# Optimization experiments

Hardware: AMD Instinct MI355X
Metric: run time of the kernel (lower is better)

## Reference

```python
import jax, jax.numpy as jnp
import numpy as np

V, E, H, B, S = 32000, 512, 1024, 128, 64
EPS = 0.05


def setup_inputs() -> dict:
    key = jax.random.key(0)
    ks = jax.random.split(key, 4)
    s = 0.02
    return {
        "emb": jax.random.normal(ks[0], (V, E), jnp.float32) * s,
        "w_ih": jax.random.normal(ks[1], (3 * H, E), jnp.float32) * s,
        "w_hh": jax.random.normal(ks[2], (3 * H, H), jnp.float32) * s,
        "b_ih": jnp.zeros((3 * H,), jnp.float32),
        "b_hh": jnp.zeros((3 * H,), jnp.float32),
        "w_dist": jax.random.normal(ks[3], (V, H), jnp.float32) * s,
        "b_dist": jnp.zeros((V,), jnp.float32),
    }


def reference(emb, w_ih, w_hh, b_ih, b_hh, w_dist, b_dist):
    base = jax.random.key(42)
    log_unif = -jnp.log(jnp.float32(V))  # log prob of uniform draw
    rows = jnp.arange(B)

    def step(carry, t):
        h, x = carry
        # PyTorch GRUCell math
        gx = x @ w_ih.T + b_ih            # [B, 3H]
        gh = h @ w_hh.T + b_hh            # [B, 3H]
        xr, xz, xn = jnp.split(gx, 3, axis=1)
        hr, hz, hn = jnp.split(gh, 3, axis=1)
        r = jax.nn.sigmoid(xr + hr)
        z = jax.nn.sigmoid(xz + hz)
        n = jnp.tanh(xn + r * hn)
        h_new = (1.0 - z) * n + z * h     # [B, H]

        dist = jax.nn.log_softmax(h_new @ w_dist.T + b_dist, axis=-1)  # [B, V]
        dist_sg = jax.lax.stop_gradient(dist)  # .detach() in torch

        k = jax.random.fold_in(base, t)
        k1, k2 = jax.random.split(k)
        # epsilon-exploration: replace whole row by uniform log-prob
        draw = jax.random.uniform(k1, (B,)) <= EPS
        dist_new = jnp.where(draw[:, None], log_unif, dist_sg)
        # Gumbel-max categorical sampling: argmax(dist_new - log(-log U))
        gumbel = -jnp.log(-jnp.log(jax.random.uniform(k2, (B, V))))
        sampled = jnp.argmax(dist_new + gumbel, axis=1)  # [B] int

        logprob = dist[rows, sampled]                                # [B]
        onp = jnp.clip(jnp.exp(dist_sg[rows, sampled]), 1e-8, 1.0)
        offp = jnp.clip(jnp.exp(dist_new[rows, sampled]), 1e-8, 1.0)
        correction = onp / offp
        prob_mean = jnp.mean(jnp.exp(dist_sg), axis=0)               # [V]

        x_next = emb[sampled]  # feed sampled token back in
        return (h_new, x_next), (sampled, correction, logprob, prob_mean)

    h0 = jnp.zeros((B, H), emb.dtype)
    x0 = jnp.broadcast_to(emb[0], (B, E))  # embedding of zero_input
    _, (samp, corr, lp, probs) = jax.lax.scan(step, (h0, x0), jnp.arange(S))
    # stack along time then transpose to [B, S] like torch.cat(..., 1)
    return samp.T, corr.T, lp.T, probs
```

## Files before the change

### kernel.cpp

```cpp
#include <hip/hip_runtime.h>
#include <cstdint>
#include <cmath>

#define V 32000
#define E 512
#define H 1024
#define B 128
#define S 64
#define NCHUNK 8
#define CHUNK 4000
#define PSTRIDE 250
#define BS (B*S)
#define PS 40
#define NEG_HUGE (-3.0e38f)

typedef __attribute__((ext_vector_type(8))) short short8;
typedef __attribute__((ext_vector_type(4))) float f32x4;

#define TFR(x0, x1, r) { x0 += x1; x1 = ((x1) << (r)) | ((x1) >> (32 - (r))); x1 ^= x0; }

__host__ __device__ inline void tf2x32(uint32_t k0, uint32_t k1, uint32_t &x0, uint32_t &x1) {
  uint32_t ks2 = k0 ^ k1 ^ 0x1BD11BDAu;
  x0 += k0; x1 += k1;
  TFR(x0,x1,13) TFR(x0,x1,15) TFR(x0,x1,26) TFR(x0,x1,6)
  x0 += k1;  x1 += ks2 + 1u;
  TFR(x0,x1,17) TFR(x0,x1,29) TFR(x0,x1,16) TFR(x0,x1,24)
  x0 += ks2; x1 += k0 + 2u;
  TFR(x0,x1,13) TFR(x0,x1,15) TFR(x0,x1,26) TFR(x0,x1,6)
  x0 += k0;  x1 += k1 + 3u;
  TFR(x0,x1,17) TFR(x0,x1,29) TFR(x0,x1,16) TFR(x0,x1,24)
  x0 += k1;  x1 += ks2 + 4u;
  TFR(x0,x1,13) TFR(x0,x1,15) TFR(x0,x1,26) TFR(x0,x1,6)
  x0 += ks2; x1 += k0 + 5u;
}

__device__ __forceinline__ uint32_t tf_bits32(uint32_t ka, uint32_t kb, uint32_t idx) {
  uint32_t x0 = 0u, x1 = idx;
  tf2x32(ka, kb, x0, x1);
  return x0 ^ x1;
}

__device__ __forceinline__ float bits_to_unif(uint32_t b) {
  return __uint_as_float((b >> 9) | 0x3f800000u) - 1.0f;
}

__device__ __forceinline__ float sigmoidf_(float x) { return 1.0f / (1.0f + expf(-x)); }

__device__ __forceinline__ ushort f2bf(float f) {
  uint32_t u = __float_as_uint(f);
  uint32_t r = u + 0x7FFFu + ((u >> 16) & 1u);
  return (ushort)(r >> 16);
}
__device__ __forceinline__ float bf2f(ushort h) { return __uint_as_float(((uint32_t)h) << 16); }

template<int BM, int BN, int BK, int TM, int TN>
__device__ void gemm_tile(const float* __restrict__ A, const float* __restrict__ Wt,
                          const float* __restrict__ bias, float* __restrict__ C,
                          int N, int K, int mblk, int nblk)
{
  constexpr int WP = BN + 4;
  __shared__ __align__(16) float As[BK][BM];
  __shared__ __align__(16) float Ws[BK][WP];
  const int tid = threadIdx.x;
  constexpr int TX = BN / TN;
  constexpr int TY = BM / TM;
  static_assert(TX * TY == 256, "bad tiling");
  const int tx = tid % TX, ty = tid / TX;
  const int n0 = tx * TN, m0 = ty * TM;

  float acc[TM][TN];
#pragma unroll
  for (int i = 0; i < TM; ++i)
#pragma unroll
    for (int j = 0; j < TN; ++j) acc[i][j] = 0.0f;

  constexpr int NA = (BM * BK / 4) / 256;
  constexpr int NW = (BN * BK / 4) / 256;
  static_assert(NA >= 1 && NW >= 1, "tile too small");

  for (int k0 = 0; k0 < K; k0 += BK) {
    __syncthreads();
#pragma unroll
    for (int q = 0; q < NA; ++q) {
      int idx = q * 256 + tid;
      int m = idx / (BK / 4), c = idx % (BK / 4);
      float4 v = *(const float4*)&A[(size_t)(mblk + m) * K + k0 + 4 * c];
      As[4*c+0][m] = v.x; As[4*c+1][m] = v.y; As[4*c+2][m] = v.z; As[4*c+3][m] = v.w;
    }
#pragma unroll
    for (int q = 0; q < NW; ++q) {
      int idx = q * 256 + tid;
      int n = idx / (BK / 4), c = idx % (BK / 4);
      float4 v = *(const float4*)&Wt[(size_t)(nblk + n) * K + k0 + 4 * c];
      Ws[4*c+0][n] = v.x; Ws[4*c+1][n] = v.y; Ws[4*c+2][n] = v.z; Ws[4*c+3][n] = v.w;
    }
    __syncthreads();
#pragma unroll
    for (int k = 0; k < BK; ++k) {
      float a[TM], w[TN];
#pragma unroll
      for (int i = 0; i < TM; ++i) a[i] = As[k][m0 + i];
#pragma unroll
      for (int j = 0; j < TN; ++j) w[j] = Ws[k][n0 + j];
#pragma unroll
      for (int i = 0; i < TM; ++i)
#pragma unroll
        for (int j = 0; j < TN; ++j) acc[i][j] += a[i] * w[j];
    }
  }
#pragma unroll
  for (int i = 0; i < TM; ++i)
#pragma unroll
    for (int j = 0; j < TN; ++j)
      C[(size_t)(mblk + m0 + i) * N + nblk + n0 + j] = acc[i][j] + bias[nblk + n0 + j];
}

__global__ __launch_bounds__(256) void gemm_dist_k(const float* __restrict__ h,
    const float* __restrict__ w_dist, const float* __restrict__ b_dist,
    float* __restrict__ logits)
{
  gemm_tile<128, 64, 16, 8, 4>(h, w_dist, b_dist, logits, V, H, 0, blockIdx.x * 64);
}

__global__ __launch_bounds__(256) void gemm_gru_k(const float* __restrict__ x,
    const float* __restrict__ h, const float* __restrict__ w_ih, const float* __restrict__ w_hh,
    const float* __restrict__ b_ih, const float* __restrict__ b_hh,
    float* __restrict__ gx, float* __restrict__ gh)
{
  int b = blockIdx.x;
  if (b < 96) {
    int rb = b & 1, cb = b >> 1;
    gemm_tile<64, 64, 16, 4, 4>(x, w_ih, b_ih, gx, 3 * H, E, rb * 64, cb * 64);
  } else {
    b -= 96;
    int rb = b & 1, cb = b >> 1;
    gemm_tile<64, 64, 16, 4, 4>(h, w_hh, b_hh, gh, 3 * H, H, rb * 64, cb * 64);
  }
}

__global__ __launch_bounds__(256) void wsplit_k(const float* __restrict__ w,
    ushort* __restrict__ whi, ushort* __restrict__ wlo, int n4)
{
  int idx = blockIdx.x * 256 + threadIdx.x;
  if (idx >= n4) return;
  size_t i = (size_t)idx * 4;
  float4 v = *(const float4*)&w[i];
  ushort h0 = f2bf(v.x), h1 = f2bf(v.y), h2 = f2bf(v.z), h3 = f2bf(v.w);
  ushort l0 = f2bf(v.x - bf2f(h0)), l1 = f2bf(v.y - bf2f(h1));
  ushort l2 = f2bf(v.z - bf2f(h2)), l3 = f2bf(v.w - bf2f(h3));
  ushort4 hv = {h0, h1, h2, h3}, lv = {l0, l1, l2, l3};
  *(ushort4*)&whi[i] = hv;
  *(ushort4*)&wlo[i] = lv;
}

__global__ __launch_bounds__(256) void gru_gates_k(const float* __restrict__ gx,
    const float* __restrict__ gh, float* __restrict__ h,
    ushort* __restrict__ hhi, ushort* __restrict__ hlo)
{
  int idx = blockIdx.x * 256 + threadIdx.x;
  int b = idx >> 10, j = idx & 1023;
  const float* gxb = gx + (size_t)b * 3 * H;
  const float* ghb = gh + (size_t)b * 3 * H;
  float r = sigmoidf_(gxb[j] + ghb[j]);
  float z = sigmoidf_(gxb[H + j] + ghb[H + j]);
  float n = tanhf(gxb[2 * H + j] + r * ghb[2 * H + j]);
  float hn = (1.0f - z) * n + z * h[idx];
  h[idx] = hn;
  ushort hi = f2bf(hn);
  hhi[idx] = hi;
  hlo[idx] = f2bf(hn - bf2f(hi));
}

__global__ __launch_bounds__(512) void gemm_dist_mfma(const ushort* __restrict__ hhi,
    const ushort* __restrict__ hlo, const ushort* __restrict__ whi,
    const ushort* __restrict__ wlo, const float* __restrict__ b_dist,
    float* __restrict__ logits,
    float* __restrict__ pm, float* __restrict__ ps,
    float* __restrict__ pbest, int* __restrict__ pidx,
    uint32_t k1a, uint32_t k1b, uint32_t k2a, uint32_t k2b)
{
  __shared__ ushort Ah[128 * PS], Al[128 * PS], Wh[128 * PS], Wl[128 * PS];
  __shared__ float rm[2 * 128], rs[2 * 128], rb_[2 * 128];
  __shared__ int   ri[2 * 128];
  __shared__ uint32_t sdraw[128];
  const int tid = threadIdx.x;
  const int wave = tid >> 6, lane = tid & 63;
  const int wm = (wave & 3) * 32;
  const int wn = (wave >> 2) * 64;
  const int nblk = blockIdx.x * 128;
  const int l15 = lane & 15;
  const int q = lane >> 4;
  const int q8 = q * 8;

  if (tid < 128)
    sdraw[tid] = (bits_to_unif(tf_bits32(k1a, k1b, (uint32_t)tid)) <= 0.05f) ? 1u : 0u;

  f32x4 acc[2][4] = {};
  const int sr = tid >> 2, sc = (tid & 3) * 8;

  for (int k0 = 0; k0 < 1024; k0 += 32) {
    __syncthreads();
    uint4 va = *(const uint4*)&hhi[(size_t)sr * 1024 + k0 + sc];
    uint4 vb = *(const uint4*)&hlo[(size_t)sr * 1024 + k0 + sc];
    uint4 vc = *(const uint4*)&whi[(size_t)(nblk + sr) * 1024 + k0 + sc];
    uint4 vd = *(const uint4*)&wlo[(size_t)(nblk + sr) * 1024 + k0 + sc];
    *(uint4*)&Ah[sr * PS + sc] = va;
    *(uint4*)&Al[sr * PS + sc] = vb;
    *(uint4*)&Wh[sr * PS + sc] = vc;
    *(uint4*)&Wl[sr * PS + sc] = vd;
    __syncthreads();

    short8 ah[2], al[2], wh[4], wl[4];
#pragma unroll
    for (int mt = 0; mt < 2; ++mt) {
      int row = wm + mt * 16 + l15;
      ah[mt] = *(const short8*)&Ah[row * PS + q8];
      al[mt] = *(const short8*)&Al[row * PS + q8];
    }
#pragma unroll
    for (int nt = 0; nt < 4; ++nt) {
      int row = wn + nt * 16 + l15;
      wh[nt] = *(const short8*)&Wh[row * PS + q8];
      wl[nt] = *(const short8*)&Wl[row * PS + q8];
    }
#pragma unroll
    for (int mt = 0; mt < 2; ++mt)
#pragma unroll
      for (int nt = 0; nt < 4; ++nt) {
        acc[mt][nt] = __builtin_amdgcn_mfma_f32_16x16x32_bf16(ah[mt], wh[nt], acc[mt][nt], 0, 0, 0);
        acc[mt][nt] = __builtin_amdgcn_mfma_f32_16x16x32_bf16(al[mt], wh[nt], acc[mt][nt], 0, 0, 0);
        acc[mt][nt] = __builtin_amdgcn_mfma_f32_16x16x32_bf16(ah[mt], wl[nt], acc[mt][nt], 0, 0, 0);
      }
  }

  float bv[4];
#pragma unroll
  for (int nt = 0; nt < 4; ++nt) bv[nt] = b_dist[nblk + wn + nt * 16 + l15];

  const float LOGU = -logf((float)V);
#pragma unroll
  for (int mt = 0; mt < 2; ++mt) {
#pragma unroll
    for (int reg = 0; reg < 4; ++reg) {
      const int r = wm + mt * 16 + q * 4 + reg;
      const bool draw = sdraw[r] != 0u;
      float m0 = NEG_HUGE, s0 = 0.0f, best = NEG_HUGE;
      int bi = 2147483647;
#pragma unroll
      for (int nt = 0; nt < 4; ++nt) {
        const int col = nblk + wn + nt * 16 + l15;
        float a = acc[mt][nt][reg] + bv[nt];
        logits[(size_t)r * V + col] = a;
        if (a > m0) { s0 = s0 * expf(m0 - a) + 1.0f; m0 = a; } else { s0 += expf(a - m0); }
        uint32_t bits = tf_bits32(k2a, k2b, (uint32_t)(r * V + col));
        float g = -logf(-logf(bits_to_unif(bits)));
        float key = draw ? (LOGU + g) : (a + g);
        if (key > best) { best = key; bi = col; }
      }
#pragma unroll
      for (int off = 1; off < 16; off <<= 1) {
        float mo = __shfl_xor(m0, off);
        float so = __shfl_xor(s0, off);
        float M = fmaxf(m0, mo);
        s0 = s0 * expf(m0 - M) + so * expf(mo - M);
        m0 = M;
        float bo = __shfl_xor(best, off);
        int io = __shfl_xor(bi, off);
        if (bo > best || (bo == best && io < bi)) { best = bo; bi = io; }
      }
      if (l15 == 0) {
        const int slot = (wave >> 2) * 128 + r;
        rm[slot] = m0; rs[slot] = s0; rb_[slot] = best; ri[slot] = bi;
      }
    }
  }
  __syncthreads();
  if (tid < 128) {
    float ma = rm[tid], sa = rs[tid], mb = rm[128 + tid], sb = rs[128 + tid];
    float M = fmaxf(ma, mb);
    float s = sa * expf(ma - M) + sb * expf(mb - M);
    pm[tid * PSTRIDE + blockIdx.x] = M;
    ps[tid * PSTRIDE + blockIdx.x] = s;
    float va = rb_[tid], vb = rb_[128 + tid];
    int ia = ri[tid], ib = ri[128 + tid];
    if (vb > va || (vb == va && ib < ia)) { va = vb; ia = ib; }
    pbest[tid * PSTRIDE + blockIdx.x] = va;
    pidx[tid * PSTRIDE + blockIdx.x] = ia;
  }
}

__device__ void gemm64_bf16x3(const ushort* __restrict__ Ahi_g, const ushort* __restrict__ Alo_g,
    const ushort* __restrict__ Whi_g, const ushort* __restrict__ Wlo_g,
    const float* __restrict__ bias, float* __restrict__ C,
    int N, int K, int mblk, int nblk)
{
  __shared__ ushort Ah[64 * PS], Al[64 * PS], Wh[64 * PS], Wl[64 * PS];
  const int tid = threadIdx.x;
  const int wave = tid >> 6, lane = tid & 63;
  const int wm = (wave & 1) * 32, wn = (wave >> 1) * 32;
  const int l15 = lane & 15, q8 = (lane >> 4) * 8;
  const int sr = tid >> 2, sc = (tid & 3) * 8;

  f32x4 acc[2][2] = {};

  for (int k0 = 0; k0 < K; k0 += 32) {
    __syncthreads();
    uint4 va = *(const uint4*)&Ahi_g[(size_t)(mblk + sr) * K + k0 + sc];
    uint4 vb = *(const uint4*)&Alo_g[(size_t)(mblk + sr) * K + k0 + sc];
    uint4 vc = *(const uint4*)&Whi_g[(size_t)(nblk + sr) * K + k0 + sc];
    uint4 vd = *(const uint4*)&Wlo_g[(size_t)(nblk + sr) * K + k0 + sc];
    *(uint4*)&Ah[sr * PS + sc] = va;
    *(uint4*)&Al[sr * PS + sc] = vb;
    *(uint4*)&Wh[sr * PS + sc] = vc;
    *(uint4*)&Wl[sr * PS + sc] = vd;
    __syncthreads();

    short8 ah[2], al[2], wh[2], wl[2];
#pragma unroll
    for (int mt = 0; mt < 2; ++mt) {
      int row = wm + mt * 16 + l15;
      ah[mt] = *(const short8*)&Ah[row * PS + q8];
      al[mt] = *(const short8*)&Al[row * PS + q8];
    }
#pragma unroll
    for (int nt = 0; nt < 2; ++nt) {
      int row = wn + nt * 16 + l15;
      wh[nt] = *(const short8*)&Wh[row * PS + q8];
      wl[nt] = *(const short8*)&Wl[row * PS + q8];
    }
#pragma unroll
    for (int mt = 0; mt < 2; ++mt)
#pragma unroll
      for (int nt = 0; nt < 2; ++nt) {
        acc[mt][nt] = __builtin_amdgcn_mfma_f32_16x16x32_bf16(ah[mt], wh[nt], acc[mt][nt], 0, 0, 0);
        acc[mt][nt] = __builtin_amdgcn_mfma_f32_16x16x32_bf16(al[mt], wh[nt], acc[mt][nt], 0, 0, 0);
        acc[mt][nt] = __builtin_amdgcn_mfma_f32_16x16x32_bf16(ah[mt], wl[nt], acc[mt][nt], 0, 0, 0);
      }
  }

#pragma unroll
  for (int nt = 0; nt < 2; ++nt) {
    int col = nblk + wn + nt * 16 + l15;
    float bv = bias[col];
#pragma unroll
    for (int mt = 0; mt < 2; ++mt) {
      int rbase = mblk + wm + mt * 16 + (lane >> 4) * 4;
#pragma unroll
      for (int reg = 0; reg < 4; ++reg)
        C[(size_t)(rbase + reg) * N + col] = acc[mt][nt][reg] + bv;
    }
  }
}

__global__ __launch_bounds__(256) void gemm_gru_mfma(
    const ushort* __restrict__ xhi, const ushort* __restrict__ xlo,
    const ushort* __restrict__ hhi, const ushort* __restrict__ hlo,
    const ushort* __restrict__ wihhi, const ushort* __restrict__ wihlo,
    const ushort* __restrict__ whhhi, const ushort* __restrict__ whhlo,
    const float* __restrict__ b_ih, const float* __restrict__ b_hh,
    float* __restrict__ gx, float* __restrict__ gh)
{
  int b = blockIdx.x;
  if (b < 96) {
    int mblk = (b & 1) * 64, nblk = (b >> 1) * 64;
    gemm64_bf16x3(xhi, xlo, wihhi, wihlo, b_ih, gx, 3 * H, E, mblk, nblk);
  } else {
    b -= 96;
    int mblk = (b & 1) * 64, nblk = (b >> 1) * 64;
    gemm64_bf16x3(hhi, hlo, whhhi, whhlo, b_hh, gh, 3 * H, H, mblk, nblk);
  }
}

__global__ __launch_bounds__(256) void init_k(const float* __restrict__ emb,
    float* __restrict__ h, float* __restrict__ x,
    ushort* __restrict__ hhi, ushort* __restrict__ hlo,
    ushort* __restrict__ xhi, ushort* __restrict__ xlo)
{
  int i = blockIdx.x * 256 + threadIdx.x;
  if (i < B * H) { h[i] = 0.0f; hhi[i] = 0; hlo[i] = 0; }
  if (i < B * E) {
    float v = emb[i & (E - 1)];
    x[i] = v;
    ushort hi = f2bf(v);
    xhi[i] = hi;
    xlo[i] = f2bf(v - bf2f(hi));
  }
}

__global__ __launch_bounds__(256) void sample_partial_k(const float* __restrict__ logits,
    float* __restrict__ pm, float* __restrict__ ps,
    float* __restrict__ pbest, int* __restrict__ pidx,
    uint32_t k1a, uint32_t k1b, uint32_t k2a, uint32_t k2b)
{
  const int b = blockIdx.x & 127, chunk = blockIdx.x >> 7;
  const int tid = threadIdx.x;
  const bool draw = bits_to_unif(tf_bits32(k1a, k1b, (uint32_t)b)) <= 0.05f;
  const float LOGU = -logf((float)V);
  const int vbeg = chunk * CHUNK, vend = vbeg + CHUNK;
  float m0 = -INFINITY, s0 = 0.0f, best = -INFINITY;
  int bi = 2147483647;
  for (int v = vbeg + tid; v < vend; v += 256) {
    float a = logits[(size_t)b * V + v];
    if (a > m0) { s0 = s0 * expf(m0 - a) + 1.0f; m0 = a; } else { s0 += expf(a - m0); }
    uint32_t bits = tf_bits32(k2a, k2b, (uint32_t)(b * V + v));
    float g = -logf(-logf(bits_to_unif(bits)));
    float key = draw ? (LOGU + g) : (a + g);
    if (key > best) { best = key; bi = v; }
  }
  __shared__ float shm[256], shs[256], sv[256];
  __shared__ int si[256];
  shm[tid] = m0; shs[tid] = s0; sv[tid] = best; si[tid] = bi;
  __syncthreads();
  for (int off = 128; off > 0; off >>= 1) {
    if (tid < off) {
      float ma = shm[tid], sa = shs[tid];
      float mb = shm[tid + off], sb = shs[tid + off];
      float M = fmaxf(ma, mb);
      shm[tid] = M;
      shs[tid] = sa * expf(ma - M) + sb * expf(mb - M);
      float va = sv[tid], vb = sv[tid + off];
      int ia = si[tid], ib = si[tid + off];
      if (vb > va || (vb == va && ib < ia)) { sv[tid] = vb; si[tid] = ib; }
    }
    __syncthreads();
  }
  if (tid == 0) {
    pm[b * PSTRIDE + chunk] = shm[0]; ps[b * PSTRIDE + chunk] = shs[0];
    pbest[b * PSTRIDE + chunk] = sv[0]; pidx[b * PSTRIDE + chunk] = si[0];
  }
}

__global__ __launch_bounds__(128) void sample_final_gather_k(const float* __restrict__ logits,
    const float* __restrict__ pm, const float* __restrict__ ps,
    const float* __restrict__ pbest, const int* __restrict__ pidx,
    float* __restrict__ rowm, float* __restrict__ rowz, int* __restrict__ samp,
    const float* __restrict__ emb, float* __restrict__ x,
    ushort* __restrict__ xhi, ushort* __restrict__ xlo,
    float* __restrict__ out, int t, uint32_t k1a, uint32_t k1b, int nchunk)
{
  __shared__ float shm[128], shs[128], shb[128];
  __shared__ int shi[128];
  __shared__ int sh_idx;
  const int b = blockIdx.x, tid = threadIdx.x;
  float m0 = NEG_HUGE, s0 = 0.0f, best = NEG_HUGE;
  int bi = 2147483647;
  for (int c = tid; c < nchunk; c += 128) {
    float ma = pm[b * PSTRIDE + c], sa = ps[b * PSTRIDE + c];
    float M = fmaxf(m0, ma);
    s0 = s0 * expf(m0 - M) + sa * expf(ma - M);
    m0 = M;
    float v = pbest[b * PSTRIDE + c];
    int ix = pidx[b * PSTRIDE + c];
    if (v > best || (v == best && ix < bi)) { best = v; bi = ix; }
  }
  shm[tid] = m0; shs[tid] = s0; shb[tid] = best; shi[tid] = bi;
  __syncthreads();
  for (int off = 64; off > 0; off >>= 1) {
    if (tid < off) {
      float ma = shm[tid], sa = shs[tid];
      float mb = shm[tid + off], sb = shs[tid + off];
      float M = fmaxf(ma, mb);
      shm[tid] = M;
      shs[tid] = sa * expf(ma - M) + sb * expf(mb - M);
      float va = shb[tid], vb = shb[tid + off];
      int ia = shi[tid], ib = shi[tid + off];
      if (vb > va || (vb == va && ib < ia)) { shb[tid] = vb; shi[tid] = ib; }
    }
    __syncthreads();
  }
  if (tid == 0) {
    float mrow = shm[0];
    float z0 = logf(shs[0]);
    int idx = shi[0];
    rowm[b] = mrow; rowz[b] = z0;
    float lp = (logits[(size_t)b * V + idx] - mrow) - z0;
    bool draw = bits_to_unif(tf_bits32(k1a, k1b, (uint32_t)b)) <= 0.05f;
    float corr = 1.0f;
    if (draw) {
      const float LOGU = -logf((float)V);
      float onp = fminf(fmaxf(expf(lp), 1e-8f), 1.0f);
      float offp = fminf(fmaxf(expf(LOGU), 1e-8f), 1.0f);
      corr = onp / offp;
    }
    out[b * S + t] = (float)idx;
    out[BS + b * S + t] = corr;
    out[2 * BS + b * S + t] = lp;
    samp[b] = idx;
    sh_idx = idx;
  }
  __syncthreads();
  const int row = sh_idx;
  float4 v = *(const float4*)&emb[(size_t)row * E + tid * 4];
  *(float4*)&x[(size_t)b * E + tid * 4] = v;
  ushort h0 = f2bf(v.x), h1 = f2bf(v.y), h2 = f2bf(v.z), h3 = f2bf(v.w);
  ushort l0 = f2bf(v.x - bf2f(h0)), l1 = f2bf(v.y - bf2f(h1));
  ushort l2 = f2bf(v.z - bf2f(h2)), l3 = f2bf(v.w - bf2f(h3));
  ushort4 hv = {h0, h1, h2, h3}, lv = {l0, l1, l2, l3};
  *(ushort4*)&xhi[(size_t)b * E + tid * 4] = hv;
  *(ushort4*)&xlo[(size_t)b * E + tid * 4] = lv;
}

__global__ __launch_bounds__(256) void probs_k(const float* __restrict__ logits,
    const float* __restrict__ rowm, const float* __restrict__ rowz,
    float* __restrict__ out, int t)
{
  __shared__ float sm[B], sz[B];
  __shared__ float red[256];
  const int tid = threadIdx.x;
  if (tid < B) { sm[tid] = rowm[tid]; sz[tid] = rowz[tid]; }
  __syncthreads();
  const int v = blockIdx.x * 64 + (tid & 63);
  const int bh = tid >> 6;
  float acc = 0.0f;
#pragma unroll 4
  for (int i = 0; i < 32; ++i) {
    int b = bh * 32 + i;
    acc += expf((logits[(size_t)b * V + v] - sm[b]) - sz[b]);
  }
  red[tid] = acc;
  __syncthreads();
  if (tid < 64) {
    float r = red[tid] + red[tid + 64] + red[tid + 128] + red[tid + 192];
    out[3 * BS + (size_t)t * V + v] = r * (1.0f / 128.0f);
  }
}

extern "C" void kernel_launch(void* const* d_in, const int* in_sizes, int n_in,
                              void* d_out, int out_size, void* d_ws, size_t ws_size,
                              hipStream_t stream) {
  (void)in_sizes; (void)n_in; (void)out_size;
  const float* emb    = (const float*)d_in[0];
  const float* w_ih   = (const float*)d_in[1];
  const float* w_hh   = (const float*)d_in[2];
  const float* b_ih   = (const float*)d_in[3];
  const float* b_hh   = (const float*)d_in[4];
  const float* w_dist = (const float*)d_in[5];
  const float* b_dist = (const float*)d_in[6];
  float* out = (float*)d_out;

  float* ws = (float*)d_ws;
  float* h      = ws;
  float* x      = h + B * H;
  float* gx     = x + B * E;
  float* gh     = gx + B * 3 * H;
  float* logits = gh + B * 3 * H;
  float* pm     = logits + (size_t)B * V;
  float* ps     = pm + B * PSTRIDE;
  float* pbest  = ps + B * PSTRIDE;
  int*   pidx   = (int*)(pbest + B * PSTRIDE);
  float* rowm   = (float*)(pidx + B * PSTRIDE);
  float* rowz   = rowm + B;
  int*   samp   = (int*)(rowz + B);
  ushort* hhi   = (ushort*)(samp + B);
  ushort* hlo   = hhi + (size_t)B * H;
  ushort* whi   = hlo + (size_t)B * H;
  ushort* wlo   = whi + (size_t)V * H;
  ushort* xhi   = wlo + (size_t)V * H;
  ushort* xlo   = xhi + (size_t)B * E;
  ushort* wihhi = xlo + (size_t)B * E;
  ushort* wihlo = wihhi + (size_t)3 * H * E;
  ushort* whhhi = wihlo + (size_t)3 * H * E;
  ushort* whhlo = whhhi + (size_t)3 * H * H;

  size_t need_dist = (size_t)((char*)xhi - (char*)d_ws);
  size_t need_gru  = (size_t)((char*)(whhlo + (size_t)3 * H * H) - (char*)d_ws);
  const bool use_dist_mfma = ws_size >= need_dist;
  const bool use_gru_mfma  = ws_size >= need_gru;

  init_k<<<512, 256, 0, stream>>>(emb, h, x, hhi, hlo, xhi, xlo);
  if (use_dist_mfma)
    wsplit_k<<<(V * H / 4 + 255) / 256, 256, 0, stream>>>(w_dist, whi, wlo, V * H / 4);
  if (use_gru_mfma) {
    wsplit_k<<<(3 * H * E / 4 + 255) / 256, 256, 0, stream>>>(w_ih, wihhi, wihlo, 3 * H * E / 4);
    wsplit_k<<<(3 * H * H / 4 + 255) / 256, 256, 0, stream>>>(w_hh, whhhi, whhlo, 3 * H * H / 4);
  }

  const uint32_t base0 = 0u, base1 = 42u;
  for (int t = 0; t < S; ++t) {
    uint32_t f0 = 0u, f1 = (uint32_t)t;
    tf2x32(base0, base1, f0, f1);
    uint32_t k1a = 0u, k1b = 0u; tf2x32(f0, f1, k1a, k1b);
    uint32_t k2a = 0u, k2b = 1u; tf2x32(f0, f1, k2a, k2b);

    if (use_gru_mfma)
      gemm_gru_mfma<<<192, 256, 0, stream>>>(xhi, xlo, hhi, hlo, wihhi, wihlo,
                                             whhhi, whhlo, b_ih, b_hh, gx, gh);
    else
      gemm_gru_k<<<192, 256, 0, stream>>>(x, h, w_ih, w_hh, b_ih, b_hh, gx, gh);
    gru_gates_k<<<512, 256, 0, stream>>>(gx, gh, h, hhi, hlo);
    int nchunk;
    if (use_dist_mfma) {
      gemm_dist_mfma<<<250, 512, 0, stream>>>(hhi, hlo, whi, wlo, b_dist, logits,
                                              pm, ps, pbest, pidx, k1a, k1b, k2a, k2b);
      nchunk = 250;
    } else {
      gemm_dist_k<<<500, 256, 0, stream>>>(h, w_dist, b_dist, logits);
      sample_partial_k<<<1024, 256, 0, stream>>>(logits, pm, ps, pbest, pidx,
                                                 k1a, k1b, k2a, k2b);
      nchunk = NCHUNK;
    }
    sample_final_gather_k<<<128, 128, 0, stream>>>(logits, pm, ps, pbest, pidx,
                                                   rowm, rowz, samp, emb, x, xhi, xlo,
                                                   out, t, k1a, k1b, nchunk);
    probs_k<<<500, 256, 0, stream>>>(logits, rowm, rowz, out, t);
  }
}
```

Measured before the change: 6.740 ms.

## Double-buffer MFMA GEMM tiles with direct global-to-LDS loads and XOR swizzle

Both bf16x3 MFMA GEMMs (the vocab projection and the GRU gates) now stage tiles with global_load_lds directly into LDS instead of going through registers. Two LDS buffers let the next K-slice load overlap the current slice's MFMAs. The padded row stride is replaced by an XOR swizzle of 8-element column groups to avoid bank conflicts. This adds LDS footprint and inline waitcnt/barrier asm, and relies on the lane-to-LDS placement of global_load_lds matching the swizzled read layout.

Result: faster. 6.269 ms (-7.0%).

```diff
diff --git a/kernel.cpp b/kernel.cpp
--- a/kernel.cpp
+++ b/kernel.cpp
@@ -11,7 +11,6 @@
 #define CHUNK 4000
 #define PSTRIDE 250
 #define BS (B*S)
-#define PS 40
 #define NEG_HUGE (-3.0e38f)
 
 typedef __attribute__((ext_vector_type(8))) short short8;
@@ -53,6 +52,11 @@
 }
 __device__ __forceinline__ float bf2f(ushort h) { return __uint_as_float(((uint32_t)h) << 16); }
 
+__device__ __forceinline__ void gload16(const ushort* g, ushort* l) {
+  __builtin_amdgcn_global_load_lds((const __attribute__((address_space(1))) void*)g,
+                                   (__attribute__((address_space(3))) void*)l, 16, 0, 0);
+}
+
 template<int BM, int BN, int BK, int TM, int TN>
 __device__ void gemm_tile(const float* __restrict__ A, const float* __restrict__ Wt,
                           const float* __restrict__ bias, float* __restrict__ C,
@@ -179,7 +183,7 @@
     float* __restrict__ pbest, int* __restrict__ pidx,
     uint32_t k1a, uint32_t k1b, uint32_t k2a, uint32_t k2b)
 {
-  __shared__ ushort Ah[128 * PS], Al[128 * PS], Wh[128 * PS], Wl[128 * PS];
+  __shared__ ushort Ah[2][128 * 32], Al[2][128 * 32], Wh[2][128 * 32], Wl[2][128 * 32];
   __shared__ float rm[2 * 128], rs[2 * 128], rb_[2 * 128];
   __shared__ int   ri[2 * 128];
   __shared__ uint32_t sdraw[128];
@@ -190,38 +194,48 @@
   const int nblk = blockIdx.x * 128;
   const int l15 = lane & 15;
   const int q = lane >> 4;
-  const int q8 = q * 8;
 
   if (tid < 128)
     sdraw[tid] = (bits_to_unif(tf_bits32(k1a, k1b, (uint32_t)tid)) <= 0.05f) ? 1u : 0u;
 
+  const int sr = tid >> 2;
+  const int gq8 = ((tid & 3) ^ ((sr >> 1) & 3)) * 8;
+  const size_t arow = (size_t)sr * 1024 + gq8;
+  const size_t wrow = (size_t)(nblk + sr) * 1024 + gq8;
+  const int wbase = wave * 512;
+
+#define DIST_STAGE(bf, kk) {                                   \
+    gload16(&hhi[arow + (kk)], &Ah[bf][wbase]);                \
+    gload16(&hlo[arow + (kk)], &Al[bf][wbase]);                \
+    gload16(&whi[wrow + (kk)], &Wh[bf][wbase]);                \
+    gload16(&wlo[wrow + (kk)], &Wl[bf][wbase]);                \
+  }
+
   f32x4 acc[2][4] = {};
-  const int sr = tid >> 2, sc = (tid & 3) * 8;
-
-  for (int k0 = 0; k0 < 1024; k0 += 32) {
-    __syncthreads();
-    uint4 va = *(const uint4*)&hhi[(size_t)sr * 1024 + k0 + sc];
-    uint4 vb = *(const uint4*)&hlo[(size_t)sr * 1024 + k0 + sc];
-    uint4 vc = *(const uint4*)&whi[(size_t)(nblk + sr) * 1024 + k0 + sc];
-    uint4 vd = *(const uint4*)&wlo[(size_t)(nblk + sr) * 1024 + k0 + sc];
-    *(uint4*)&Ah[sr * PS + sc] = va;
-    *(uint4*)&Al[sr * PS + sc] = vb;
-    *(uint4*)&Wh[sr * PS + sc] = vc;
-    *(uint4*)&Wl[sr * PS + sc] = vd;
-    __syncthreads();
+
+  DIST_STAGE(0, 0);
+  asm volatile("s_waitcnt vmcnt(0)" ::: "memory");
+  __builtin_amdgcn_sched_barrier(0);
+  __builtin_amdgcn_s_barrier();
+
+  int buf = 0;
+  for (int k0 = 0; k0 < 1024; k0 += 32, buf ^= 1) {
+    if (k0 + 32 < 1024) DIST_STAGE(buf ^ 1, k0 + 32);
 
     short8 ah[2], al[2], wh[4], wl[4];
 #pragma unroll
     for (int mt = 0; mt < 2; ++mt) {
       int row = wm + mt * 16 + l15;
-      ah[mt] = *(const short8*)&Ah[row * PS + q8];
-      al[mt] = *(const short8*)&Al[row * PS + q8];
+      int off = row * 32 + ((q ^ ((row >> 1) & 3)) * 8);
+      ah[mt] = *(const short8*)&Ah[buf][off];
+      al[mt] = *(const short8*)&Al[buf][off];
     }
 #pragma unroll
     for (int nt = 0; nt < 4; ++nt) {
       int row = wn + nt * 16 + l15;
-      wh[nt] = *(const short8*)&Wh[row * PS + q8];
-      wl[nt] = *(const short8*)&Wl[row * PS + q8];
+      int off = row * 32 + ((q ^ ((row >> 1) & 3)) * 8);
+      wh[nt] = *(const short8*)&Wh[buf][off];
+      wl[nt] = *(const short8*)&Wl[buf][off];
     }
 #pragma unroll
     for (int mt = 0; mt < 2; ++mt)
@@ -231,7 +245,12 @@
         acc[mt][nt] = __builtin_amdgcn_mfma_f32_16x16x32_bf16(al[mt], wh[nt], acc[mt][nt], 0, 0, 0);
         acc[mt][nt] = __builtin_amdgcn_mfma_f32_16x16x32_bf16(ah[mt], wl[nt], acc[mt][nt], 0, 0, 0);
       }
-  }
+
+    asm volatile("s_waitcnt vmcnt(0)" ::: "memory");
+    __builtin_amdgcn_sched_barrier(0);
+    __builtin_amdgcn_s_barrier();
+  }
+#undef DIST_STAGE
 
   float bv[4];
 #pragma unroll
@@ -294,39 +313,50 @@
     const float* __restrict__ bias, float* __restrict__ C,
     int N, int K, int mblk, int nblk)
 {
-  __shared__ ushort Ah[64 * PS], Al[64 * PS], Wh[64 * PS], Wl[64 * PS];
+  __shared__ ushort Ah[2][64 * 32], Al[2][64 * 32], Wh[2][64 * 32], Wl[2][64 * 32];
   const int tid = threadIdx.x;
   const int wave = tid >> 6, lane = tid & 63;
   const int wm = (wave & 1) * 32, wn = (wave >> 1) * 32;
-  const int l15 = lane & 15, q8 = (lane >> 4) * 8;
-  const int sr = tid >> 2, sc = (tid & 3) * 8;
+  const int l15 = lane & 15, q = lane >> 4;
+
+  const int sr = tid >> 2;
+  const int gq8 = ((tid & 3) ^ ((sr >> 1) & 3)) * 8;
+  const size_t arow = (size_t)(mblk + sr) * K + gq8;
+  const size_t wrow = (size_t)(nblk + sr) * K + gq8;
+  const int wbase = wave * 512;
+
+#define GRU_STAGE(bf, kk) {                                    \
+    gload16(&Ahi_g[arow + (kk)], &Ah[bf][wbase]);              \
+    gload16(&Alo_g[arow + (kk)], &Al[bf][wbase]);              \
+    gload16(&Whi_g[wrow + (kk)], &Wh[bf][wbase]);              \
+    gload16(&Wlo_g[wrow + (kk)], &Wl[bf][wbase]);              \
+  }
 
   f32x4 acc[2][2] = {};
 
-  for (int k0 = 0; k0 < K; k0 += 32) {
-    __syncthreads();
-    uint4 va = *(const uint4*)&Ahi_g[(size_t)(mblk + sr) * K + k0 + sc];
-    uint4 vb = *(const uint4*)&Alo_g[(size_t)(mblk + sr) * K + k0 + sc];
-    uint4 vc = *(const uint4*)&Whi_g[(size_t)(nblk + sr) * K + k0 + sc];
-    uint4 vd = *(const uint4*)&Wlo_g[(size_t)(nblk + sr) * K + k0 + sc];
-    *(uint4*)&Ah[sr * PS + sc] = va;
-    *(uint4*)&Al[sr * PS + sc] = vb;
-    *(uint4*)&Wh[sr * PS + sc] = vc;
-    *(uint4*)&Wl[sr * PS + sc] = vd;
-    __syncthreads();
+  GRU_STAGE(0, 0);
+  asm volatile("s_waitcnt vmcnt(0)" ::: "memory");
+  __builtin_amdgcn_sched_barrier(0);
+  __builtin_amdgcn_s_barrier();
+
+  int buf = 0;
+  for (int k0 = 0; k0 < K; k0 += 32, buf ^= 1) {
+    if (k0 + 32 < K) GRU_STAGE(buf ^ 1, k0 + 32);
 
     short8 ah[2], al[2], wh[2], wl[2];
 #pragma unroll
     for (int mt = 0; mt < 2; ++mt) {
       int row = wm + mt * 16 + l15;
-      ah[mt] = *(const short8*)&Ah[row * PS + q8];
-      al[mt] = *(const short8*)&Al[row * PS + q8];
+      int off = row * 32 + ((q ^ ((row >> 1) & 3)) * 8);
+      ah[mt] = *(const short8*)&Ah[buf][off];
+      al[mt] = *(const short8*)&Al[buf][off];
     }
 #pragma unroll
     for (int nt = 0; nt < 2; ++nt) {
       int row = wn + nt * 16 + l15;
-      wh[nt] = *(const short8*)&Wh[row * PS + q8];
-      wl[nt] = *(const short8*)&Wl[row * PS + q8];
+      int off = row * 32 + ((q ^ ((row >> 1) & 3)) * 8);
+      wh[nt] = *(const short8*)&Wh[buf][off];
+      wl[nt] = *(const short8*)&Wl[buf][off];
     }
 #pragma unroll
     for (int mt = 0; mt < 2; ++mt)
@@ -336,7 +366,12 @@
         acc[mt][nt] = __builtin_amdgcn_mfma_f32_16x16x32_bf16(al[mt], wh[nt], acc[mt][nt], 0, 0, 0);
         acc[mt][nt] = __builtin_amdgcn_mfma_f32_16x16x32_bf16(ah[mt], wl[nt], acc[mt][nt], 0, 0, 0);
       }
-  }
+
+    asm volatile("s_waitcnt vmcnt(0)" ::: "memory");
+    __builtin_amdgcn_sched_barrier(0);
+    __builtin_amdgcn_s_barrier();
+  }
+#undef GRU_STAGE
 
 #pragma unroll
   for (int nt = 0; nt < 2; ++nt) {
```
